# Kernel tuning notes

Hardware: AMD Instinct MI355X
Metric: run time of the kernel (lower is better)

The kernel has to match this reference:

```python
import jax, jax.numpy as jnp
import numpy as np
import math

HEAD_DIM = 128
N_HEADS = 32
N_KV_HEADS = 8
ROPE_THETA = 10000.0


def _rotate_half(x):
    x1, x2 = jnp.split(x, 2, axis=-1)
    return jnp.concatenate([-x2, x1], axis=-1)


def _rope_cos_sin(position_ids, head_dim, theta):
    # position_ids: [B, S] int
    inv_freq = 1.0 / (theta ** (jnp.arange(0, head_dim, 2, dtype=jnp.float32) / head_dim))
    freqs = position_ids.astype(jnp.float32)[..., None] * inv_freq[None, None, :]  # [B,S,D/2]
    emb = jnp.concatenate([freqs, freqs], axis=-1)  # [B,S,D]
    return jnp.cos(emb), jnp.sin(emb)


def setup_inputs() -> dict:
    key = jax.random.key(0)
    k1, k2, k3, k4, k5 = jax.random.split(key, 5)
    B, S, H = 1, 2048, 4096
    hidden_states = jax.random.normal(k1, (B, S, H), dtype=jnp.float32)
    Wq = jax.random.normal(k2, (N_HEADS * HEAD_DIM, H), dtype=jnp.float32) * (1.0 / math.sqrt(H))
    Wk = jax.random.normal(k3, (N_KV_HEADS * HEAD_DIM, H), dtype=jnp.float32) * (1.0 / math.sqrt(H))
    Wv = jax.random.normal(k4, (N_KV_HEADS * HEAD_DIM, H), dtype=jnp.float32) * (1.0 / math.sqrt(H))
    Wo = jax.random.normal(k5, (H, N_HEADS * HEAD_DIM), dtype=jnp.float32) * (1.0 / math.sqrt(H))
    position_ids = jnp.arange(S, dtype=jnp.int32)[None, :]
    return {"hidden_states": hidden_states, "Wq": Wq, "Wk": Wk, "Wv": Wv, "Wo": Wo,
            "position_ids": position_ids}


def reference(hidden_states, Wq, Wk, Wv, Wo, position_ids):
    B, S, H = hidden_states.shape
    d = HEAD_DIM
    groups = N_HEADS // N_KV_HEADS

    # projections (torch Linear: x @ W^T)
    q = (hidden_states @ Wq.T).reshape(B, S, N_HEADS, d).transpose(0, 2, 1, 3)      # [B,Hq,S,d]
    k = (hidden_states @ Wk.T).reshape(B, S, N_KV_HEADS, d).transpose(0, 2, 1, 3)   # [B,Hk,S,d]
    v = (hidden_states @ Wv.T).reshape(B, S, N_KV_HEADS, d).transpose(0, 2, 1, 3)

    cos, sin = _rope_cos_sin(position_ids, d, ROPE_THETA)  # [B,S,d]
    cos = cos[:, None, :, :]
    sin = sin[:, None, :, :]
    q = q * cos + _rotate_half(q) * sin
    k = k * cos + _rotate_half(k) * sin

    # GQA: repeat kv heads
    k = jnp.repeat(k, groups, axis=1)  # [B,Hq,S,d]
    v = jnp.repeat(v, groups, axis=1)

    scores = jnp.einsum('bhqd,bhkd->bhqk', q, k) / math.sqrt(d)
    causal = jnp.tril(jnp.ones((S, S), dtype=bool))
    scores = jnp.where(causal[None, None], scores, jnp.finfo(jnp.float32).min)
    attn = jax.nn.softmax(scores.astype(jnp.float32), axis=-1).astype(q.dtype)

    out = jnp.einsum('bhqk,bhkd->bhqd', attn, v)        # [B,Hq,S,d]
    out = out.transpose(0, 2, 1, 3).reshape(B, S, N_HEADS * d)
    return out @ Wo.T
```

## Files before the change

### kernel.cpp

```cpp
#include <hip/hip_runtime.h>
#include <hip/hip_bf16.h>
#include <cstdint>
#include <cstddef>

#define S_LEN 2048
#define HID   4096
#define HD    128
#define NH    32
#define NKV   8
#define KVW   (NKV * HD)
#define QKVN  (HID + 2 * KVW)

typedef __bf16 bf16x8_t __attribute__((ext_vector_type(8)));
typedef float  f32x4_t  __attribute__((ext_vector_type(4)));
typedef unsigned short u16x8_t __attribute__((ext_vector_type(8)));

__device__ __forceinline__ unsigned short f2b(float f) {
  unsigned u = __float_as_uint(f);
  u += 0x7FFFu + ((u >> 16) & 1u);
  return (unsigned short)(u >> 16);
}
__device__ __forceinline__ float b2f(unsigned short v) {
  return __uint_as_float(((unsigned)v) << 16);
}
__device__ __forceinline__ void gld_lds16(const void* g, void* l) {
  __builtin_amdgcn_global_load_lds(
      (const __attribute__((address_space(1))) void*)g,
      (__attribute__((address_space(3))) void*)l, 16, 0, 0);
}

__global__ void cvt_kernel(const float* __restrict__ src,
                           unsigned short* __restrict__ dst, int n4) {
  int i = blockIdx.x * blockDim.x + threadIdx.x;
  int stride = gridDim.x * blockDim.x;
  for (; i < n4; i += stride) {
    float4 v = reinterpret_cast<const float4*>(src)[i];
    ushort4 o;
    o.x = f2b(v.x); o.y = f2b(v.y); o.z = f2b(v.z); o.w = f2b(v.w);
    reinterpret_cast<ushort4*>(dst)[i] = o;
  }
}

__global__ void rope_kernel(unsigned short* __restrict__ Q,
                            unsigned short* __restrict__ Kb,
                            const int* __restrict__ pos_ids) {
  const int total = S_LEN * (NH + NKV) * 64;
  int idx = blockIdx.x * blockDim.x + threadIdx.x;
  int stride = gridDim.x * blockDim.x;
  for (; idx < total; idx += stride) {
    int s   = idx / ((NH + NKV) * 64);
    int rem = idx % ((NH + NKV) * 64);
    int hp  = rem >> 6;
    int i   = rem & 63;
    unsigned short* ptr; int W, h;
    if (hp < NH) { ptr = Q;  W = HID; h = hp; }
    else         { ptr = Kb; W = KVW; h = hp - NH; }
    float pos = (float)pos_ids[s];
    float ang = pos * __expf(-(float)i * 0.14391156516f);
    float sn, cs;
    sincosf(ang, &sn, &cs);
    size_t base = (size_t)s * W + (size_t)h * HD + i;
    float lo = b2f(ptr[base]);
    float hi = b2f(ptr[base + 64]);
    ptr[base]      = f2b(lo * cs - hi * sn);
    ptr[base + 64] = f2b(hi * cs + lo * sn);
  }
}

template <int BN, int MODE>
__global__ __launch_bounds__(256, 2) void gemm4w_kernel(
    const unsigned short* __restrict__ A, const unsigned short* __restrict__ B,
    void* __restrict__ C0, void* __restrict__ C1, void* __restrict__ C2,
    int N, int K) {
  constexpr int NFRW = BN / 32;
  constexpr int ABYTES = 128 * 128;
  constexpr int TILE_LDS = ABYTES + BN * 128;
  __shared__ char ldsB[2 * TILE_LDS];

  const int tid  = threadIdx.x;
  const int lane = tid & 63;
  const int wid  = tid >> 6;
  const int wm = wid >> 1, wn = wid & 1;
  const int lr = lane & 15, g = lane >> 4;
  const int bm = blockIdx.y * 128;
  const int bn = blockIdx.x * BN;
  const int nk = K >> 6;
  const int ni = nk >> 1;
  const int xr = (lr & 7) << 4;

  auto stage_u = [&](int t, int u) {
    if (t >= nk) return;
    const int riu = tid >> 3;
    const int cbs = ((tid & 7) << 4) ^ ((riu & 7) << 4);
    const char* src;
    if (u < 4)
      src = (const char*)A + ((size_t)(bm + u * 32 + riu) * K + t * 64) * 2 + cbs;
    else
      src = (const char*)B + ((size_t)(bn + (u - 4) * 32 + riu) * K + t * 64) * 2 + cbs;
    gld_lds16(src, ldsB + (t & 1) * TILE_LDS + u * 4096 + tid * 16);
  };

  auto rdA = [&](const char* bb, int m, int k) {
    const int row = wm * 64 + m * 16 + lr;
    return *(const bf16x8_t*)(bb + row * 128 + ((k * 64 + g * 16) ^ xr));
  };
  auto rdB = [&](const char* bb, int n, int k) {
    const int row = wn * (BN / 2) + n * 16 + lr;
    return *(const bf16x8_t*)(bb + ABYTES + row * 128 + ((k * 64 + g * 16) ^ xr));
  };

  for (int t = 0; t < 2; ++t)
    for (int u = 0; u < 4 + NFRW; ++u) stage_u(t, u);
  asm volatile("s_waitcnt vmcnt(0)" ::: "memory");
  __builtin_amdgcn_sched_barrier(0);
  __builtin_amdgcn_s_barrier();

  f32x4_t acc[4][NFRW];
#pragma unroll
  for (int m = 0; m < 4; ++m)
#pragma unroll
    for (int n = 0; n < NFRW; ++n) acc[m][n] = f32x4_t{0.f, 0.f, 0.f, 0.f};

  bf16x8_t bfr[NFRW][2], af[2][2];

#define MFMA_BLOCK(MB)                                                        \
  __builtin_amdgcn_s_setprio(1);                                              \
  _Pragma("unroll") for (int m = 0; m < 2; ++m)                               \
    _Pragma("unroll") for (int n = 0; n < NFRW; ++n)                          \
      _Pragma("unroll") for (int k = 0; k < 2; ++k)                           \
        acc[(MB) + m][n] = __builtin_amdgcn_mfma_f32_16x16x32_bf16(           \
            af[m][k], bfr[n][k], acc[(MB) + m][n], 0, 0, 0);                  \
  __builtin_amdgcn_s_setprio(0);

#define GATE()                                                                \
  __builtin_amdgcn_s_barrier();                                               \
  asm volatile("s_waitcnt lgkmcnt(0)" ::: "memory");                          \
  __builtin_amdgcn_sched_barrier(0);

#define RD_A2(bb, m0)                                                         \
  _Pragma("unroll") for (int m = 0; m < 2; ++m)                               \
    _Pragma("unroll") for (int k = 0; k < 2; ++k)                             \
      af[m][k] = rdA(bb, (m0) + m, k);

#define RD_B(bb)                                                              \
  _Pragma("unroll") for (int n = 0; n < NFRW; ++n)                            \
    _Pragma("unroll") for (int k = 0; k < 2; ++k)                             \
      bfr[n][k] = rdB(bb, n, k);

  for (int i = 0; i < ni; ++i) {
    const char* bE = ldsB;
    const char* bO = ldsB + TILE_LDS;
    const int tO = 2 * i + 1, tE2 = 2 * i + 2, tO2 = 2 * i + 3;
    const bool last = (i == ni - 1);

    RD_B(bE);
    RD_A2(bE, 0);
    if (i > 0) {
#pragma unroll
      for (int u = 0; u < 4; ++u) stage_u(tO, u);
    }
    GATE(); MFMA_BLOCK(0);
    __builtin_amdgcn_s_barrier();

    RD_A2(bE, 2);
#pragma unroll
    for (int u = 0; u < NFRW; ++u) stage_u(tE2, 4 + u);
    GATE(); MFMA_BLOCK(2);
    if (last) { asm volatile("s_waitcnt vmcnt(0)" ::: "memory"); }
    else      { asm volatile("s_waitcnt vmcnt(%0)" :: "n"(NFRW) : "memory"); }
    __builtin_amdgcn_sched_barrier(0);
    __builtin_amdgcn_s_barrier();

    RD_B(bO);
    RD_A2(bO, 0);
#pragma unroll
    for (int u = 0; u < 4; ++u) stage_u(tE2, u);
    GATE(); MFMA_BLOCK(0);
    __builtin_amdgcn_s_barrier();

    RD_A2(bO, 2);
#pragma unroll
    for (int u = 0; u < NFRW; ++u) stage_u(tO2, 4 + u);
    GATE(); MFMA_BLOCK(2);
    if (!last) { asm volatile("s_waitcnt vmcnt(%0)" :: "n"(NFRW) : "memory"); }
    __builtin_amdgcn_sched_barrier(0);
    __builtin_amdgcn_s_barrier();
  }
#undef MFMA_BLOCK
#undef GATE
#undef RD_A2
#undef RD_B

#pragma unroll
  for (int mf = 0; mf < 4; ++mf) {
    const int row0 = bm + wm * 64 + mf * 16 + g * 4;
#pragma unroll
    for (int nf = 0; nf < NFRW; ++nf) {
      const int col = bn + wn * (BN / 2) + nf * 16 + lr;
      if constexpr (MODE == 1) {
#pragma unroll
        for (int r = 0; r < 4; ++r)
          ((float*)C0)[(size_t)(row0 + r) * N + col] = acc[mf][nf][r];
      } else {
        if (col < HID) {
#pragma unroll
          for (int r = 0; r < 4; ++r)
            ((unsigned short*)C0)[(size_t)(row0 + r) * HID + col] = f2b(acc[mf][nf][r]);
        } else if (col < HID + KVW) {
#pragma unroll
          for (int r = 0; r < 4; ++r)
            ((unsigned short*)C1)[(size_t)(row0 + r) * KVW + (col - HID)] = f2b(acc[mf][nf][r]);
        } else {
          const int c2 = col - HID - KVW;
          ushort4 w;
          w.x = f2b(acc[mf][nf][0]); w.y = f2b(acc[mf][nf][1]);
          w.z = f2b(acc[mf][nf][2]); w.w = f2b(acc[mf][nf][3]);
          *(ushort4*)(void*)&((unsigned short*)C2)[(size_t)c2 * S_LEN + row0] = w;
        }
      }
    }
  }
}

__global__ __launch_bounds__(256) void attn_kernel(
    const unsigned short* __restrict__ Q, const unsigned short* __restrict__ K,
    const unsigned short* __restrict__ VtG, unsigned short* __restrict__ O,
    const float* __restrict__ WoF, unsigned short* __restrict__ WoB) {
  __shared__ char KlB[2][16384];
  __shared__ char VtB2[2][16384];
  __shared__ unsigned short Pl[4][16][72];

  const int tid  = threadIdx.x;
  const int lane = tid & 63;
  const int wave = tid >> 6;
  const int h    = blockIdx.y;
  const int kvh  = h >> 2;
  const int pair = blockIdx.x;
  const int lr   = lane & 15;
  const int g    = lane >> 4;
  const int lk8  = g * 8;
  const float scale = 0.08838834764831845f;
  const int blkl = h * 16 + pair;
  const int CVT_LIM = (HID * HID) / 4;
  int itg = 0;
  int pendidx = 0x7FFFFFFF;
  float4 pend;

  auto stageK = [&](int kv0, int buf) {
#pragma unroll
    for (int j = 0; j < 4; ++j) {
      const int row  = j * 16 + (tid >> 4);
      const int colb = ((tid & 15) << 4) ^ ((row & 15) << 4);
      const char* src =
          (const char*)(K + (size_t)(kv0 + row) * KVW + (size_t)kvh * HD) + colb;
      gld_lds16(src, &KlB[buf][row * 256 + ((tid & 15) << 4)]);
    }
  };
  auto stageV = [&](int kv0, int buf) {
#pragma unroll
    for (int j = 0; j < 4; ++j) {
      const int row  = j * 32 + (tid >> 3);
      const int colb = ((tid & 7) << 4) ^ ((row & 7) << 4);
      const char* src =
          (const char*)(VtG + ((size_t)kvh * HD + row) * S_LEN + kv0) + colb;
      gld_lds16(src, &VtB2[buf][row * 128 + ((tid & 7) << 4)]);
    }
  };
  auto rdK = [&](int buf, int n, int c) {
    const int row = n * 16 + lr;
    return *(const bf16x8_t*)&KlB[buf][row * 256 +
                                       ((c * 64 + g * 16) ^ ((lr & 15) << 4))];
  };
  auto rdV = [&](int buf, int c, int half) {
    const int row = c * 16 + lr;
    return *(const bf16x8_t*)&VtB2[buf][row * 128 +
                                        ((half * 64 + g * 16) ^ ((lr & 7) << 4))];
  };

  for (int pass = 0; pass < 2; ++pass) {
    const int qb = pass == 0 ? (31 - pair) : pair;
    const int q0 = qb * 64;
    const int qrow = q0 + wave * 16;
    const int nkv = qb + 1;

    bf16x8_t qf[4];
    {
      const unsigned short* qp = Q + (size_t)(qrow + lr) * HID + (size_t)h * HD;
#pragma unroll
      for (int c = 0; c < 4; ++c)
        qf[c] = *(const bf16x8_t*)(const void*)(qp + c * 32 + lk8);
    }
    f32x4_t oacc[8];
#pragma unroll
    for (int c = 0; c < 8; ++c) oacc[c] = f32x4_t{0.f, 0.f, 0.f, 0.f};
    float m_run = -3e38f, l_run = 0.f;

    stageK(0, 0); stageV(0, 0);
    asm volatile("s_waitcnt vmcnt(0)" ::: "memory");
    __builtin_amdgcn_sched_barrier(0);
    __builtin_amdgcn_s_barrier();

    for (int it = 0; it < nkv; ++it) {
      const int kv0 = it * 64;
      const int buf = it & 1;

      if (pendidx < CVT_LIM) {
        ushort4 o;
        o.x = f2b(pend.x); o.y = f2b(pend.y);
        o.z = f2b(pend.z); o.w = f2b(pend.w);
        reinterpret_cast<ushort4*>(WoB)[pendidx] = o;
      }
      pendidx = (blkl * 33 + itg) * 256 + tid;
      ++itg;
      if (pendidx < CVT_LIM)
        pend = reinterpret_cast<const float4*>(WoF)[pendidx];

      if (it + 1 < nkv) { stageK(kv0 + 64, buf ^ 1); stageV(kv0 + 64, buf ^ 1); }

      f32x4_t sacc[4];
#pragma unroll
      for (int n = 0; n < 4; ++n) sacc[n] = f32x4_t{0.f, 0.f, 0.f, 0.f};
#pragma unroll
      for (int c = 0; c < 4; ++c) {
        bf16x8_t qc = qf[c];
#pragma unroll
        for (int n = 0; n < 4; ++n)
          sacc[n] = __builtin_amdgcn_mfma_f32_16x16x32_bf16(rdK(buf, n, c), qc,
                                                            sacc[n], 0, 0, 0);
      }

      const int qg = qrow + lr;
      const bool diag = (it == nkv - 1);
      float p[16];
      float mloc = -3e38f;
#pragma unroll
      for (int n = 0; n < 4; ++n)
#pragma unroll
        for (int r = 0; r < 4; ++r) {
          float x = sacc[n][r] * scale;
          if (diag) {
            int kg = kv0 + n * 16 + g * 4 + r;
            if (kg > qg) x = -3e38f;
          }
          p[n * 4 + r] = x;
          mloc = fmaxf(mloc, x);
        }
      mloc = fmaxf(mloc, __shfl_xor(mloc, 16));
      mloc = fmaxf(mloc, __shfl_xor(mloc, 32));

      if (__any(mloc > m_run + 8.f)) {
        float m_new = fmaxf(m_run, mloc);
        float alpha = __expf(m_run - m_new);
        float a4[4];
#pragma unroll
        for (int r = 0; r < 4; ++r) a4[r] = __shfl(alpha, g * 4 + r);
#pragma unroll
        for (int c = 0; c < 8; ++c)
#pragma unroll
          for (int r = 0; r < 4; ++r) oacc[c][r] *= a4[r];
        l_run *= alpha;
        m_run = m_new;
      }

      float ssum = 0.f;
#pragma unroll
      for (int i = 0; i < 16; ++i) {
        float e = __expf(p[i] - m_run);
        p[i] = e;
        ssum += e;
      }
      ssum += __shfl_xor(ssum, 16);
      ssum += __shfl_xor(ssum, 32);
      l_run += ssum;

#pragma unroll
      for (int n = 0; n < 4; ++n) {
        ushort4 w;
        w.x = f2b(p[n * 4 + 0]); w.y = f2b(p[n * 4 + 1]);
        w.z = f2b(p[n * 4 + 2]); w.w = f2b(p[n * 4 + 3]);
        *(ushort4*)(void*)&Pl[wave][lr][n * 16 + g * 4] = w;
      }

#pragma unroll
      for (int half = 0; half < 2; ++half) {
        bf16x8_t pf = *(const bf16x8_t*)(const void*)&Pl[wave][lr][half * 32 + lk8];
#pragma unroll
        for (int c = 0; c < 8; ++c)
          oacc[c] = __builtin_amdgcn_mfma_f32_16x16x32_bf16(pf, rdV(buf, c, half),
                                                            oacc[c], 0, 0, 0);
      }

      if (it + 1 < nkv) { asm volatile("s_waitcnt vmcnt(0)" ::: "memory"); }
      __builtin_amdgcn_sched_barrier(0);
      __builtin_amdgcn_s_barrier();
    }

    float linv[4];
#pragma unroll
    for (int r = 0; r < 4; ++r) linv[r] = 1.f / __shfl(l_run, g * 4 + r);
#pragma unroll
    for (int r = 0; r < 4; ++r) {
      int row = qrow + g * 4 + r;
#pragma unroll
      for (int c = 0; c < 8; ++c)
        O[(size_t)row * HID + (size_t)h * HD + c * 16 + lr] = f2b(oacc[c][r] * linv[r]);
    }
  }

  if (pendidx < CVT_LIM) {
    ushort4 o;
    o.x = f2b(pend.x); o.y = f2b(pend.y);
    o.z = f2b(pend.z); o.w = f2b(pend.w);
    reinterpret_cast<ushort4*>(WoB)[pendidx] = o;
  }
}

extern "C" void kernel_launch(void* const* d_in, const int* in_sizes, int n_in,
                              void* d_out, int out_size, void* d_ws, size_t ws_size,
                              hipStream_t stream) {
  (void)in_sizes; (void)n_in; (void)out_size; (void)ws_size;
  const float* X  = (const float*)d_in[0];
  const float* Wq = (const float*)d_in[1];
  const float* Wk = (const float*)d_in[2];
  const float* Wv = (const float*)d_in[3];
  const float* Wo = (const float*)d_in[4];
  const int*  pos = (const int*)d_in[5];
  float* out = (float*)d_out;

  unsigned short* Xb  = (unsigned short*)d_ws;
  unsigned short* Wqb = Xb  + (size_t)S_LEN * HID;
  unsigned short* Wkb = Wqb + (size_t)HID * HID;
  unsigned short* Wvb = Wkb + (size_t)KVW * HID;
  unsigned short* Wob = Wvb + (size_t)KVW * HID;
  unsigned short* Qb  = Wob + (size_t)HID * HID;
  unsigned short* Kb  = Qb  + (size_t)S_LEN * HID;
  unsigned short* VtB = Kb  + (size_t)S_LEN * KVW;
  unsigned short* AOb = VtB + (size_t)S_LEN * KVW;

  auto cvt = [&](const float* s, unsigned short* d, size_t n) {
    int n4 = (int)(n / 4);
    int grid = (n4 + 255) / 256;
    if (grid > 4096) grid = 4096;
    cvt_kernel<<<grid, 256, 0, stream>>>(s, d, n4);
  };
  cvt(X,  Xb,  (size_t)S_LEN * HID);
  cvt(Wq, Wqb, (size_t)HID * HID);
  cvt(Wk, Wkb, (size_t)KVW * HID);
  cvt(Wv, Wvb, (size_t)KVW * HID);

  gemm4w_kernel<192, 2><<<dim3(QKVN / 192, S_LEN / 128), 256, 0, stream>>>(
      Xb, Wqb, Qb, Kb, VtB, QKVN, HID);

  rope_kernel<<<2048, 256, 0, stream>>>(Qb, Kb, pos);

  attn_kernel<<<dim3(16, NH), 256, 0, stream>>>(Qb, Kb, VtB, AOb, Wo, Wob);

  gemm4w_kernel<128, 1><<<dim3(HID / 128, S_LEN / 128), 256, 0, stream>>>(
      AOb, Wob, out, nullptr, nullptr, HID, HID);
}
```

Before: 283.0 us.

## Add 8-wave pipelined QKV GEMM and fold softmax scale into RoPE

Replaces the QKV projection GEMM with a new 512-thread, 8-wave kernel that splits each K-step into half-blocks. Loads for the next tiles are interleaved with MFMA blocks using barriers, setprio and vmcnt gating, so memory latency overlaps compute. It also premultiplies Q by scale*log2(e) in the RoPE kernel, which lets attention drop its per-score multiply and use exp2f in place of __expf. The changes add scheduling complexity and extra barriers, and rounding the scaled Q to bf16 slightly changes precision.

New measurement: 289.3 us. +2.2%, slower.

```diff
diff --git a/kernel.cpp b/kernel.cpp
--- a/kernel.cpp
+++ b/kernel.cpp
@@ -41,6 +41,7 @@
   }
 }
 
+#define QSCALE 0.12751744846f
 __global__ void rope_kernel(unsigned short* __restrict__ Q,
                             unsigned short* __restrict__ Kb,
                             const int* __restrict__ pos_ids) {
@@ -62,8 +63,162 @@
     size_t base = (size_t)s * W + (size_t)h * HD + i;
     float lo = b2f(ptr[base]);
     float hi = b2f(ptr[base + 64]);
-    ptr[base]      = f2b(lo * cs - hi * sn);
-    ptr[base + 64] = f2b(hi * cs + lo * sn);
+    float o0 = lo * cs - hi * sn;
+    float o1 = hi * cs + lo * sn;
+    if (hp < NH) { o0 *= QSCALE; o1 *= QSCALE; }
+    ptr[base]      = f2b(o0);
+    ptr[base + 64] = f2b(o1);
+  }
+}
+
+template <int BN, int MODE>
+__global__ __launch_bounds__(512, 4) void gemm4p_kernel(
+    const unsigned short* __restrict__ A, const unsigned short* __restrict__ B,
+    void* __restrict__ C0, void* __restrict__ C1, void* __restrict__ C2,
+    int N, int K) {
+  constexpr int NFR = BN / 64;
+  constexpr int ABYTES = 128 * 128;
+  constexpr int TILE_LDS = ABYTES + BN * 128;
+  __shared__ char ldsB[2 * TILE_LDS];
+
+  const int tid  = threadIdx.x;
+  const int lane = tid & 63;
+  const int wid  = tid >> 6;
+  const int wm = wid >> 2, wn = wid & 3;
+  const int lr = lane & 15, g = lane >> 4;
+  const int bm = blockIdx.y * 128;
+  const int bn = blockIdx.x * BN;
+  const int nk = K >> 6;
+  const int ni = nk >> 1;
+  const int xr = (lr & 7) << 4;
+
+  auto stage_u = [&](int t, int u) {
+    if (t >= nk) return;
+    const int riu = tid >> 3;
+    const int cbs = ((tid & 7) << 4) ^ ((riu & 7) << 4);
+    const char* src;
+    if (u < 2)
+      src = (const char*)A + ((size_t)(bm + u * 64 + riu) * K + t * 64) * 2 + cbs;
+    else
+      src = (const char*)B + ((size_t)(bn + (u - 2) * 64 + riu) * K + t * 64) * 2 + cbs;
+    gld_lds16(src, ldsB + (t & 1) * TILE_LDS + u * 8192 + tid * 16);
+  };
+
+  auto rdA = [&](const char* bb, int m, int k) {
+    const int row = wm * 64 + m * 16 + lr;
+    return *(const bf16x8_t*)(bb + row * 128 + ((k * 64 + g * 16) ^ xr));
+  };
+  auto rdB = [&](const char* bb, int n, int k) {
+    const int row = wn * (BN / 4) + n * 16 + lr;
+    return *(const bf16x8_t*)(bb + ABYTES + row * 128 + ((k * 64 + g * 16) ^ xr));
+  };
+
+  for (int t = 0; t < 2; ++t)
+    for (int u = 0; u < 2 + NFR; ++u) stage_u(t, u);
+  asm volatile("s_waitcnt vmcnt(0)" ::: "memory");
+  __builtin_amdgcn_sched_barrier(0);
+  __builtin_amdgcn_s_barrier();
+
+  f32x4_t acc[4][NFR];
+#pragma unroll
+  for (int m = 0; m < 4; ++m)
+#pragma unroll
+    for (int n = 0; n < NFR; ++n) acc[m][n] = f32x4_t{0.f, 0.f, 0.f, 0.f};
+
+  bf16x8_t bfr[NFR][2], af[2][2];
+
+#define MFMA_BLOCK(MB)                                                        \
+  __builtin_amdgcn_s_setprio(1);                                              \
+  _Pragma("unroll") for (int m = 0; m < 2; ++m)                               \
+    _Pragma("unroll") for (int n = 0; n < NFR; ++n)                           \
+      _Pragma("unroll") for (int k = 0; k < 2; ++k)                           \
+        acc[(MB) + m][n] = __builtin_amdgcn_mfma_f32_16x16x32_bf16(           \
+            af[m][k], bfr[n][k], acc[(MB) + m][n], 0, 0, 0);                  \
+  __builtin_amdgcn_s_setprio(0);
+
+#define GATE()                                                                \
+  __builtin_amdgcn_s_barrier();                                               \
+  asm volatile("s_waitcnt lgkmcnt(0)" ::: "memory");                          \
+  __builtin_amdgcn_sched_barrier(0);
+
+#define RD_A2(bb, m0)                                                         \
+  _Pragma("unroll") for (int m = 0; m < 2; ++m)                               \
+    _Pragma("unroll") for (int k = 0; k < 2; ++k)                             \
+      af[m][k] = rdA(bb, (m0) + m, k);
+
+#define RD_B(bb)                                                              \
+  _Pragma("unroll") for (int n = 0; n < NFR; ++n)                             \
+    _Pragma("unroll") for (int k = 0; k < 2; ++k)                             \
+      bfr[n][k] = rdB(bb, n, k);
+
+  for (int i = 0; i < ni; ++i) {
+    const char* bE = ldsB;
+    const char* bO = ldsB + TILE_LDS;
+    const int tO = 2 * i + 1, tE2 = 2 * i + 2, tO2 = 2 * i + 3;
+    const bool last = (i == ni - 1);
+
+    RD_B(bE);
+    RD_A2(bE, 0);
+    if (i > 0) { stage_u(tO, 0); stage_u(tO, 1); }
+    GATE(); MFMA_BLOCK(0);
+    __builtin_amdgcn_s_barrier();
+
+    RD_A2(bE, 2);
+#pragma unroll
+    for (int u = 0; u < NFR; ++u) stage_u(tE2, 2 + u);
+    GATE(); MFMA_BLOCK(2);
+    if (last) { asm volatile("s_waitcnt vmcnt(0)" ::: "memory"); }
+    else      { asm volatile("s_waitcnt vmcnt(%0)" :: "n"(NFR) : "memory"); }
+    __builtin_amdgcn_sched_barrier(0);
+    __builtin_amdgcn_s_barrier();
+
+    RD_B(bO);
+    RD_A2(bO, 0);
+    stage_u(tE2, 0); stage_u(tE2, 1);
+    GATE(); MFMA_BLOCK(0);
+    __builtin_amdgcn_s_barrier();
+
+    RD_A2(bO, 2);
+#pragma unroll
+    for (int u = 0; u < NFR; ++u) stage_u(tO2, 2 + u);
+    GATE(); MFMA_BLOCK(2);
+    if (!last) { asm volatile("s_waitcnt vmcnt(%0)" :: "n"(NFR) : "memory"); }
+    __builtin_amdgcn_sched_barrier(0);
+    __builtin_amdgcn_s_barrier();
+  }
+#undef MFMA_BLOCK
+#undef GATE
+#undef RD_A2
+#undef RD_B
+
+#pragma unroll
+  for (int mf = 0; mf < 4; ++mf) {
+    const int row0 = bm + wm * 64 + mf * 16 + g * 4;
+#pragma unroll
+    for (int nf = 0; nf < NFR; ++nf) {
+      const int col = bn + wn * (BN / 4) + nf * 16 + lr;
+      if constexpr (MODE == 1) {
+#pragma unroll
+        for (int r = 0; r < 4; ++r)
+          ((float*)C0)[(size_t)(row0 + r) * N + col] = acc[mf][nf][r];
+      } else {
+        if (col < HID) {
+#pragma unroll
+          for (int r = 0; r < 4; ++r)
+            ((unsigned short*)C0)[(size_t)(row0 + r) * HID + col] = f2b(acc[mf][nf][r]);
+        } else if (col < HID + KVW) {
+#pragma unroll
+          for (int r = 0; r < 4; ++r)
+            ((unsigned short*)C1)[(size_t)(row0 + r) * KVW + (col - HID)] = f2b(acc[mf][nf][r]);
+        } else {
+          const int c2 = col - HID - KVW;
+          ushort4 w;
+          w.x = f2b(acc[mf][nf][0]); w.y = f2b(acc[mf][nf][1]);
+          w.z = f2b(acc[mf][nf][2]); w.w = f2b(acc[mf][nf][3]);
+          *(ushort4*)(void*)&((unsigned short*)C2)[(size_t)c2 * S_LEN + row0] = w;
+        }
+      }
+    }
   }
 }
 
@@ -239,7 +394,6 @@
   const int lr   = lane & 15;
   const int g    = lane >> 4;
   const int lk8  = g * 8;
-  const float scale = 0.08838834764831845f;
   const int blkl = h * 16 + pair;
   const int CVT_LIM = (HID * HID) / 4;
   int itg = 0;
@@ -337,7 +491,7 @@
       for (int n = 0; n < 4; ++n)
 #pragma unroll
         for (int r = 0; r < 4; ++r) {
-          float x = sacc[n][r] * scale;
+          float x = sacc[n][r];
           if (diag) {
             int kg = kv0 + n * 16 + g * 4 + r;
             if (kg > qg) x = -3e38f;
@@ -350,7 +504,7 @@
 
       if (__any(mloc > m_run + 8.f)) {
         float m_new = fmaxf(m_run, mloc);
-        float alpha = __expf(m_run - m_new);
+        float alpha = exp2f(m_run - m_new);
         float a4[4];
 #pragma unroll
         for (int r = 0; r < 4; ++r) a4[r] = __shfl(alpha, g * 4 + r);
@@ -365,7 +519,7 @@
       float ssum = 0.f;
 #pragma unroll
       for (int i = 0; i < 16; ++i) {
-        float e = __expf(p[i] - m_run);
+        float e = exp2f(p[i] - m_run);
         p[i] = e;
         ssum += e;
       }
@@ -448,7 +602,7 @@
   cvt(Wk, Wkb, (size_t)KVW * HID);
   cvt(Wv, Wvb, (size_t)KVW * HID);
 
-  gemm4w_kernel<192, 2><<<dim3(QKVN / 192, S_LEN / 128), 256, 0, stream>>>(
+  gemm4p_kernel<192, 2><<<dim3(QKVN / 192, S_LEN / 128), 512, 0, stream>>>(
       Xb, Wqb, Qb, Kb, VtB, QKVN, HID);
 
   rope_kernel<<<2048, 256, 0, stream>>>(Qb, Kb, pos);
```
